# Optimization experiments

Measured on AMD Instinct MI355X. Metric: run time of the kernel, lower is better.

Reference implementation:

```python
import jax, jax.numpy as jnp
import numpy as np

B, T, D = 4, 2048, 1024
F = 4 * D  # Config.RWKV_INTERMIDATE_SIZE * hidden_dim
LN_EPS = 1e-3  # keras LayerNormalization default epsilon


def layer_norm(x, g, b, eps=LN_EPS):
    mu = jnp.mean(x, axis=-1, keepdims=True)
    var = jnp.mean(jnp.square(x - mu), axis=-1, keepdims=True)
    return (x - mu) * jax.lax.rsqrt(var + eps) * g + b


def setup_inputs() -> dict:
    ks = jax.random.split(jax.random.key(0), 24)
    g = lambda k, shape: (jax.random.normal(k, shape, jnp.float32)
                          * np.sqrt(2.0 / sum(shape)))  # ~glorot
    return {
        "x": jax.random.normal(ks[0], (B, T, D), jnp.float32),
        "s_cm": jnp.zeros((B, D), jnp.float32),
        "s_tm": jnp.zeros((B, D), jnp.float32),
        "s_num": jnp.zeros((B, D), jnp.float32),
        "s_den": jnp.zeros((B, D), jnp.float32),
        "s_q": jnp.zeros((B, D), jnp.float32),
        "ln1_g": jnp.ones((D,), jnp.float32),
        "ln1_b": jnp.zeros((D,), jnp.float32),
        "ln2_g": jnp.ones((D,), jnp.float32),
        "ln2_b": jnp.zeros((D,), jnp.float32),
        "tm_mix_k": jax.random.uniform(ks[1], (D,), jnp.float32, 0.0, 2.0 / D),
        "tm_mix_v": jax.random.uniform(ks[2], (D,), jnp.float32, 0.0, 2.0 / D),
        "tm_mix_r": jax.random.uniform(ks[3], (D,), jnp.float32, 0.0, (2.0 / D) ** 0.5),
        "tm_kw": g(ks[4], (D, D)),
        "tm_vw": g(ks[5], (D, D)),
        "tm_rw": g(ks[6], (D, D)),
        "time_decay": jax.random.uniform(ks[7], (D,), jnp.float32, 0.0, 0.1),
        "time_first": jax.random.uniform(ks[8], (D,), jnp.float32, 0.0, 0.05),
        "out_w": g(ks[9], (D, D)),
        "cm_mix_k": jax.random.uniform(ks[10], (D,), jnp.float32, 0.0, 2.0 / D),
        "cm_mix_r": jax.random.uniform(ks[11], (D,), jnp.float32, 0.0, 2.0 / D),
        "cm_kw": g(ks[12], (D, F)),
        "cm_vw": g(ks[13], (F, D)),
        "cm_rw": g(ks[14], (D, D)),
    }


def _shift(h, s):
    # token shift: prepend last-token state, drop last timestep
    return jnp.concatenate([s[:, None, :], h[:, :-1, :]], axis=1)


def reference(x, s_cm, s_tm, s_num, s_den, s_q,
              ln1_g, ln1_b, ln2_g, ln2_b,
              tm_mix_k, tm_mix_v, tm_mix_r, tm_kw, tm_vw, tm_rw,
              time_decay, time_first, out_w,
              cm_mix_k, cm_mix_r, cm_kw, cm_vw, cm_rw):
    # ---- time mixing ----
    h = layer_norm(x, ln1_g, ln1_b)  # [B,T,D]
    hs = _shift(h, s_tm)
    xk = h * tm_mix_k + hs * (1.0 - tm_mix_k)
    xv = h * tm_mix_v + hs * (1.0 - tm_mix_v)
    xr = h * tm_mix_r + hs * (1.0 - tm_mix_r)
    k = xk @ tm_kw  # [B,T,D]
    v = xv @ tm_vw
    r = jax.nn.sigmoid(xr @ tm_rw)
    w = -jnp.exp(time_decay)  # [D]

    def step(carry, kv):
        num, den, q = carry
        kt, vt = kv  # [B,D]
        mo = jnp.maximum(q, kt + time_first)
        e1 = jnp.exp(q - mo)
        e2 = jnp.exp(kt + time_first - mo)
        out = (e1 * num + e2 * vt) / (e1 * den + e2)
        ms = jnp.maximum(q + w, kt)
        e1s = jnp.exp(q + w - ms)
        e2s = jnp.exp(kt - ms)
        return (e1s * num + e2s * vt, e1s * den + e2s, ms), out

    (num, den, q), wkv = jax.lax.scan(
        step, (s_num, s_den, s_q),
        (k.transpose(1, 0, 2), v.transpose(1, 0, 2)))
    wkv = wkv.transpose(1, 0, 2)  # [B,T,D]
    x = x + (r * wkv) @ out_w

    # ---- channel mixing ----
    h2 = layer_norm(x, ln2_g, ln2_b)
    hs2 = _shift(h2, s_cm)
    xk2 = h2 * cm_mix_k + hs2 * (1.0 - cm_mix_k)
    xr2 = h2 * cm_mix_r + hs2 * (1.0 - cm_mix_r)
    kv = jnp.square(jax.nn.relu(xk2 @ cm_kw)) @ cm_vw  # [B,T,F] -> [B,T,D]
    x = x + jax.nn.sigmoid(xr2 @ cm_rw) * kv

    # new state: (cm_inputs, tm_inputs, num, den, q)
    return x, h2[:, -1], h[:, -1], num, den, q
```

## Files before the change

### kernel.cpp

```cpp
#include <hip/hip_runtime.h>

typedef unsigned short ushort_t;
typedef __attribute__((ext_vector_type(8))) short short8;
typedef __attribute__((ext_vector_type(4))) float f32x4;

#define B_ 4
#define T_ 2048
#define D_ 1024
#define F_ 4096
#define M_ (B_*T_)
#define CH_ 64
#define NC_ (T_/CH_)

#define AS1 __attribute__((address_space(1)))
#define AS3 __attribute__((address_space(3)))

__device__ __forceinline__ ushort_t f2bf(float f) {
  union { float f; unsigned u; } a; a.f = f;
  unsigned r = a.u + 0x7FFFu + ((a.u >> 16) & 1u);
  return (ushort_t)(r >> 16);
}

__device__ __forceinline__ float bf2f(ushort_t u) {
  union { unsigned u; float f; } a; a.u = ((unsigned)u) << 16;
  return a.f;
}

__device__ __forceinline__ void gl_lds16(const void* g, void* l) {
  __builtin_amdgcn_global_load_lds((AS1 void*)(__UINTPTR_TYPE__)g,
                                   (AS3 void*)l, 16, 0, 0);
}

__device__ __forceinline__ void xcd_swz(int gx, int gy, int& bx, int& by, int& bz) {
  int lid = blockIdx.x + gx * (blockIdx.y + gy * blockIdx.z);
  int nwg = gx * gy * gridDim.z;
  int cpx = nwg >> 3;
  int L = (lid & 7) * cpx + (lid >> 3);
  by = L % gy;
  int t1 = L / gy;
  bx = t1 % gx;
  bz = t1 / gx;
}

__global__ __launch_bounds__(256) void tconv(const float* __restrict__ W,
                                             ushort_t* __restrict__ Wt,
                                             int K, int N) {
  __shared__ float tile[32][33];
  int tx = threadIdx.x, ty = threadIdx.y;
  int n0 = blockIdx.x * 32, k0 = blockIdx.y * 32;
  #pragma unroll
  for (int i = 0; i < 32; i += 8)
    tile[ty + i][tx] = W[(size_t)(k0 + ty + i) * N + n0 + tx];
  __syncthreads();
  #pragma unroll
  for (int i = 0; i < 32; i += 8)
    Wt[(size_t)(n0 + ty + i) * K + k0 + tx] = f2bf(tile[tx][ty + i]);
}

__global__ __launch_bounds__(256) void tconv5(const float* __restrict__ s0,
                                              const float* __restrict__ s1,
                                              const float* __restrict__ s2,
                                              const float* __restrict__ s3,
                                              const float* __restrict__ s4,
                                              ushort_t* __restrict__ d0,
                                              ushort_t* __restrict__ d1,
                                              ushort_t* __restrict__ d2,
                                              ushort_t* __restrict__ d3,
                                              ushort_t* __restrict__ d4) {
  __shared__ float tile[32][33];
  int z = blockIdx.z;
  const float* W = (z == 0) ? s0 : (z == 1) ? s1 : (z == 2) ? s2 : (z == 3) ? s3 : s4;
  ushort_t* Wt   = (z == 0) ? d0 : (z == 1) ? d1 : (z == 2) ? d2 : (z == 3) ? d3 : d4;
  int tx = threadIdx.x, ty = threadIdx.y;
  int n0 = blockIdx.x * 32, k0 = blockIdx.y * 32;
  #pragma unroll
  for (int i = 0; i < 32; i += 8)
    tile[ty + i][tx] = W[(size_t)(k0 + ty + i) * D_ + n0 + tx];
  __syncthreads();
  #pragma unroll
  for (int i = 0; i < 32; i += 8)
    Wt[(size_t)(n0 + ty + i) * D_ + k0 + tx] = f2bf(tile[tx][ty + i]);
}

#define MIX1(c, p, f) f2bf((c) * (f) + (p) * (1.0f - (f)))

template <int NOUT>
__global__ __launch_bounds__(256)
void ln_mix(const float* __restrict__ xin, const float* __restrict__ st,
            const float* __restrict__ g, const float* __restrict__ bb,
            const float* __restrict__ mk, const float* __restrict__ mv,
            const float* __restrict__ mr,
            ushort_t* __restrict__ ok, ushort_t* __restrict__ ov,
            ushort_t* __restrict__ orr, float* __restrict__ last) {
  int row = blockIdx.x;
  int t = row & (T_ - 1);
  int b = row >> 11;
  int tid = threadIdx.x;
  const bool pln = (t != 0);
  float4 vc = ((const float4*)(xin + (size_t)row * D_))[tid];
  float4 vp = pln ? ((const float4*)(xin + (size_t)(row - 1) * D_))[tid]
                  : ((const float4*)(st + (size_t)b * D_))[tid];
  float s0 = vc.x + vc.y + vc.z + vc.w;
  float s1 = vc.x * vc.x + vc.y * vc.y + vc.z * vc.z + vc.w * vc.w;
  float s2 = vp.x + vp.y + vp.z + vp.w;
  float s3 = vp.x * vp.x + vp.y * vp.y + vp.z * vp.z + vp.w * vp.w;
  #pragma unroll
  for (int o = 32; o > 0; o >>= 1) {
    s0 += __shfl_down(s0, o); s1 += __shfl_down(s1, o);
    s2 += __shfl_down(s2, o); s3 += __shfl_down(s3, o);
  }
  __shared__ float red[4][4];
  if ((tid & 63) == 0) {
    int w = tid >> 6;
    red[w][0] = s0; red[w][1] = s1; red[w][2] = s2; red[w][3] = s3;
  }
  __syncthreads();
  float cs0 = red[0][0] + red[1][0] + red[2][0] + red[3][0];
  float cs1 = red[0][1] + red[1][1] + red[2][1] + red[3][1];
  float ps0 = red[0][2] + red[1][2] + red[2][2] + red[3][2];
  float ps1 = red[0][3] + red[1][3] + red[2][3] + red[3][3];

  float mu = cs0 * (1.0f / D_);
  float rs = rsqrtf(cs1 * (1.0f / D_) - mu * mu + 1e-3f);
  float4 gv = ((const float4*)g)[tid];
  float4 bv = ((const float4*)bb)[tid];
  float hc[4], hp[4];
  hc[0] = (vc.x - mu) * rs * gv.x + bv.x;
  hc[1] = (vc.y - mu) * rs * gv.y + bv.y;
  hc[2] = (vc.z - mu) * rs * gv.z + bv.z;
  hc[3] = (vc.w - mu) * rs * gv.w + bv.w;
  if (pln) {
    float mup = ps0 * (1.0f / D_);
    float rsp = rsqrtf(ps1 * (1.0f / D_) - mup * mup + 1e-3f);
    hp[0] = (vp.x - mup) * rsp * gv.x + bv.x;
    hp[1] = (vp.y - mup) * rsp * gv.y + bv.y;
    hp[2] = (vp.z - mup) * rsp * gv.z + bv.z;
    hp[3] = (vp.w - mup) * rsp * gv.w + bv.w;
  } else {
    hp[0] = vp.x; hp[1] = vp.y; hp[2] = vp.z; hp[3] = vp.w;
  }

  size_t qi = (size_t)row * 256 + tid;
  float4 k4 = ((const float4*)mk)[tid];
  float4 r4 = ((const float4*)mr)[tid];
  ushort4 o4;
  o4.x = MIX1(hc[0], hp[0], k4.x); o4.y = MIX1(hc[1], hp[1], k4.y);
  o4.z = MIX1(hc[2], hp[2], k4.z); o4.w = MIX1(hc[3], hp[3], k4.w);
  ((ushort4*)ok)[qi] = o4;
  if (NOUT == 3) {
    float4 v4 = ((const float4*)mv)[tid];
    o4.x = MIX1(hc[0], hp[0], v4.x); o4.y = MIX1(hc[1], hp[1], v4.y);
    o4.z = MIX1(hc[2], hp[2], v4.z); o4.w = MIX1(hc[3], hp[3], v4.w);
    ((ushort4*)ov)[qi] = o4;
  }
  o4.x = MIX1(hc[0], hp[0], r4.x); o4.y = MIX1(hc[1], hp[1], r4.y);
  o4.z = MIX1(hc[2], hp[2], r4.z); o4.w = MIX1(hc[3], hp[3], r4.w);
  ((ushort4*)orr)[qi] = o4;

  if (t == T_ - 1) {
    float4 h4; h4.x = hc[0]; h4.y = hc[1]; h4.z = hc[2]; h4.w = hc[3];
    ((float4*)(last + (size_t)b * D_))[tid] = h4;
  }
}

__global__ __launch_bounds__(256) void wkv_part1(const ushort_t* __restrict__ k,
                                                 const ushort_t* __restrict__ v,
                                                 const float* __restrict__ tdec,
                                                 float* __restrict__ cn,
                                                 float* __restrict__ cd,
                                                 float* __restrict__ cq) {
  int idx = blockIdx.x * 256 + threadIdx.x;
  int d = idx & (D_ - 1);
  int b = (idx >> 10) & (B_ - 1);
  int c = idx >> 12;
  float w = -__expf(tdec[d]);
  const ushort_t* kp = k + ((size_t)b * T_ + c * CH_) * D_ + d;
  const ushort_t* vp = v + ((size_t)b * T_ + c * CH_) * D_ + d;
  float num = 0.0f, den = 0.0f, q = -1e30f;
  for (int t0 = 0; t0 < CH_; t0 += 8) {
    float kt[8], vt[8];
    #pragma unroll
    for (int i = 0; i < 8; ++i) {
      size_t off = (size_t)(t0 + i) * D_;
      kt[i] = bf2f(kp[off]); vt[i] = bf2f(vp[off]);
    }
    #pragma unroll
    for (int i = 0; i < 8; ++i) {
      float kk = kt[i];
      float ms = fmaxf(q + w, kk);
      float e1 = __expf(q + w - ms), e2 = __expf(kk - ms);
      num = e1 * num + e2 * vt[i];
      den = e1 * den + e2;
      q = ms;
    }
  }
  cn[idx] = num; cd[idx] = den; cq[idx] = q;
}

__global__ __launch_bounds__(256) void wkv_part2(const float* __restrict__ cn,
                                                 const float* __restrict__ cd,
                                                 const float* __restrict__ cq,
                                                 const float* __restrict__ sn,
                                                 const float* __restrict__ sd,
                                                 const float* __restrict__ sq,
                                                 const float* __restrict__ tdec,
                                                 float* __restrict__ pn,
                                                 float* __restrict__ pd,
                                                 float* __restrict__ pq,
                                                 float* __restrict__ on,
                                                 float* __restrict__ od,
                                                 float* __restrict__ oq) {
  int idx = blockIdx.x * 256 + threadIdx.x;
  int d = idx & (D_ - 1);
  float w = -__expf(tdec[d]);
  float wL = w * (float)CH_;
  float num = sn[idx], den = sd[idx], q = sq[idx];
  #pragma unroll 4
  for (int c = 0; c < NC_; ++c) {
    int j = (c << 12) + idx;
    pn[j] = num; pd[j] = den; pq[j] = q;
    float m2 = cq[j];
    float qn = fmaxf(q + wL, m2);
    float e1 = __expf(q + wL - qn), e2 = __expf(m2 - qn);
    num = e1 * num + e2 * cn[j];
    den = e1 * den + e2 * cd[j];
    q = qn;
  }
  on[idx] = num; od[idx] = den; oq[idx] = q;
}

__global__ __launch_bounds__(256) void wkv_part3(const ushort_t* __restrict__ k,
                                                 const ushort_t* __restrict__ v,
                                                 const ushort_t* __restrict__ r,
                                                 const float* __restrict__ pn,
                                                 const float* __restrict__ pd,
                                                 const float* __restrict__ pq,
                                                 const float* __restrict__ tdec,
                                                 const float* __restrict__ tfirst,
                                                 ushort_t* __restrict__ rwkv) {
  int idx = blockIdx.x * 256 + threadIdx.x;
  int d = idx & (D_ - 1);
  int b = (idx >> 10) & (B_ - 1);
  int c = idx >> 12;
  float w = -__expf(tdec[d]);
  float tf = tfirst[d];
  float num = pn[idx], den = pd[idx], q = pq[idx];
  size_t base = ((size_t)b * T_ + c * CH_) * D_ + d;
  const ushort_t* kp = k + base;
  const ushort_t* vp = v + base;
  const ushort_t* rp = r + base;
  ushort_t* op = rwkv + base;
  for (int t0 = 0; t0 < CH_; t0 += 8) {
    float kt[8], vt[8], rt[8];
    #pragma unroll
    for (int i = 0; i < 8; ++i) {
      size_t off = (size_t)(t0 + i) * D_;
      kt[i] = bf2f(kp[off]); vt[i] = bf2f(vp[off]); rt[i] = bf2f(rp[off]);
    }
    #pragma unroll
    for (int i = 0; i < 8; ++i) {
      float kk = kt[i];
      float mo = fmaxf(q, kk + tf);
      float e1 = __expf(q - mo), e2 = __expf(kk + tf - mo);
      float o = (e1 * num + e2 * vt[i]) / (e1 * den + e2);
      op[(size_t)(t0 + i) * D_] = f2bf(rt[i] * o);
      float ms = fmaxf(q + w, kk);
      float e1s = __expf(q + w - ms), e2s = __expf(kk - ms);
      num = e1s * num + e2s * vt[i];
      den = e1s * den + e2s;
      q = ms;
    }
  }
}

template <int EPI>
__global__ __launch_bounds__(512, 2)
void gemm256(const ushort_t* __restrict__ A, const ushort_t* __restrict__ Bt,
             int N, int K, int ktn, ushort_t* __restrict__ Cb) {
  __shared__ alignas(16) ushort_t sA[2][256 * 64];
  __shared__ alignas(16) ushort_t sB[2][256 * 64];
  const int tid = threadIdx.x;
  const int lane = tid & 63;
  const int wave = tid >> 6;
  const int wr = wave >> 2, wc = wave & 3;
  const int l15 = lane & 15;
  const int kb = (lane >> 4) << 4;
  int bx, by, bz;
  xcd_swz(gridDim.x, gridDim.y, bx, by, bz);
  const int m0 = bx * 256, n0 = by * 256;
  const ushort_t* gA = A + (size_t)m0 * K;
  const ushort_t* gB = Bt + (size_t)n0 * K;

  const int sr = tid >> 3;
  const int sc8 = (tid & 7) ^ (sr & 7);
  const int scb = (tid & 7) * 16;

  auto stage = [&](int dbuf, int kt, int h) {
    const ushort_t* g = (h < 2) ? gA : gB;
    ushort_t* sb = (h < 2) ? sA[dbuf] : sB[dbuf];
    int rbase = (h & 1) * 128;
    #pragma unroll
    for (int i = 0; i < 2; ++i) {
      int row = rbase + i * 64 + sr;
      gl_lds16(g + (size_t)row * K + (size_t)kt * 64 + sc8 * 8,
               (char*)sb + row * 128 + scb);
    }
  };

  auto ld = [&](const ushort_t* sbuf, int row, int s5) -> short8 {
    int cb = ((s5 << 6) + kb) ^ ((row & 7) << 4);
    return *(const short8*)((const char*)sbuf + row * 128 + cb);
  };

  f32x4 acc[8][4] = {};

  stage(0, 0, 0); stage(0, 0, 1); stage(0, 0, 2); stage(0, 0, 3);

  for (int t = 0; t < ktn; ++t) {
    const int cur = t & 1, nxt = cur ^ 1;
    const bool more = (t + 1 < ktn);
    if (more) { stage(nxt, t + 1, 0); stage(nxt, t + 1, 1); }
    if (more) asm volatile("s_waitcnt vmcnt(4)" ::: "memory");
    else      asm volatile("s_waitcnt vmcnt(0)" ::: "memory");
    __builtin_amdgcn_s_barrier();

    const ushort_t* curA = sA[cur];
    const ushort_t* curB = sB[cur];
    short8 bfr[4][2];

#define G256_MFMA16(MI0, A00, A01, A10, A11)                                  \
    __builtin_amdgcn_s_setprio(1);                                            \
    _Pragma("unroll")                                                         \
    for (int ni = 0; ni < 4; ++ni) {                                          \
      acc[MI0][ni] = __builtin_amdgcn_mfma_f32_16x16x32_bf16(                 \
          A00, bfr[ni][0], acc[MI0][ni], 0, 0, 0);                            \
      acc[MI0][ni] = __builtin_amdgcn_mfma_f32_16x16x32_bf16(                 \
          A01, bfr[ni][1], acc[MI0][ni], 0, 0, 0);                            \
      acc[MI0 + 1][ni] = __builtin_amdgcn_mfma_f32_16x16x32_bf16(             \
          A10, bfr[ni][0], acc[MI0 + 1][ni], 0, 0, 0);                        \
      acc[MI0 + 1][ni] = __builtin_amdgcn_mfma_f32_16x16x32_bf16(             \
          A11, bfr[ni][1], acc[MI0 + 1][ni], 0, 0, 0);                        \
    }                                                                         \
    __builtin_amdgcn_s_setprio(0);

#define G256_SYNC_IN()                                                        \
    asm volatile("" ::: "memory");                                            \
    __builtin_amdgcn_s_barrier();                                             \
    asm volatile("s_waitcnt lgkmcnt(0)" ::: "memory");                        \
    __builtin_amdgcn_sched_barrier(0);

#define G256_SYNC_OUT()                                                       \
    asm volatile("" ::: "memory");                                            \
    __builtin_amdgcn_s_barrier();

    {
      #pragma unroll
      for (int ni = 0; ni < 4; ++ni)
        #pragma unroll
        for (int s = 0; s < 2; ++s)
          bfr[ni][s] = ld(curB, wc * 64 + ni * 16 + l15, s);
      short8 a00 = ld(curA, wr * 128 + 0 * 16 + l15, 0);
      short8 a01 = ld(curA, wr * 128 + 0 * 16 + l15, 1);
      short8 a10 = ld(curA, wr * 128 + 1 * 16 + l15, 0);
      short8 a11 = ld(curA, wr * 128 + 1 * 16 + l15, 1);
      if (more) stage(nxt, t + 1, 2);
      G256_SYNC_IN();
      G256_MFMA16(0, a00, a01, a10, a11);
      G256_SYNC_OUT();
    }
    {
      short8 a00 = ld(curA, wr * 128 + 2 * 16 + l15, 0);
      short8 a01 = ld(curA, wr * 128 + 2 * 16 + l15, 1);
      short8 a10 = ld(curA, wr * 128 + 3 * 16 + l15, 0);
      short8 a11 = ld(curA, wr * 128 + 3 * 16 + l15, 1);
      if (more) stage(nxt, t + 1, 3);
      G256_SYNC_IN();
      G256_MFMA16(2, a00, a01, a10, a11);
      G256_SYNC_OUT();
    }
    {
      short8 a00 = ld(curA, wr * 128 + 4 * 16 + l15, 0);
      short8 a01 = ld(curA, wr * 128 + 4 * 16 + l15, 1);
      short8 a10 = ld(curA, wr * 128 + 5 * 16 + l15, 0);
      short8 a11 = ld(curA, wr * 128 + 5 * 16 + l15, 1);
      G256_SYNC_IN();
      G256_MFMA16(4, a00, a01, a10, a11);
      G256_SYNC_OUT();
    }
    {
      short8 a00 = ld(curA, wr * 128 + 6 * 16 + l15, 0);
      short8 a01 = ld(curA, wr * 128 + 6 * 16 + l15, 1);
      short8 a10 = ld(curA, wr * 128 + 7 * 16 + l15, 0);
      short8 a11 = ld(curA, wr * 128 + 7 * 16 + l15, 1);
      G256_SYNC_IN();
      G256_MFMA16(6, a00, a01, a10, a11);
      G256_SYNC_OUT();
    }
  }

  #pragma unroll
  for (int mi = 0; mi < 8; ++mi)
    #pragma unroll
    for (int ni = 0; ni < 4; ++ni)
      #pragma unroll
      for (int j = 0; j < 4; ++j) {
        int row = m0 + wr * 128 + mi * 16 + ((lane >> 4) << 2) + j;
        int col = n0 + wc * 64 + ni * 16 + l15;
        size_t idx = (size_t)row * N + col;
        float v = acc[mi][ni][j];
        float tt = v > 0.0f ? v : 0.0f;
        Cb[idx] = f2bf(tt * tt);
      }
}

template <int EPI>
__global__ __launch_bounds__(512, 2)
void gemmB(const ushort_t* __restrict__ A, const ushort_t* __restrict__ Bt,
           int K, int ktn,
           float* __restrict__ Cf, ushort_t* __restrict__ Ub,
           const float* __restrict__ X, const float* __restrict__ X2) {
  __shared__ alignas(16) ushort_t sA[2][128 * 64];
  __shared__ alignas(16) ushort_t sB[2][256 * 64];
  const int tid = threadIdx.x;
  const int lane = tid & 63;
  const int wave = tid >> 6;
  const int wr = wave >> 2, wc = wave & 3;
  const int l15 = lane & 15;
  const int kb = (lane >> 4) << 4;
  int bx, by, zid;
  xcd_swz(gridDim.x, gridDim.y, bx, by, zid);
  const int m0 = bx * 128, n0 = by * 256;

  const ushort_t* Ause = A;
  const ushort_t* Buse = Bt;
  if (EPI == 3) {
    Ause = A + (size_t)zid * M_ * D_;
    Buse = Bt + (size_t)zid * D_ * D_;
  }
  const ushort_t* gA = Ause + (size_t)m0 * K;
  const ushort_t* gB = Buse + (size_t)n0 * K;

  const int sr = tid >> 3;
  const int sc8 = (tid & 7) ^ (sr & 7);
  const int scb = (tid & 7) * 16;

  auto stage = [&](int dbuf, int kt, int h) {
    if (h < 2) {
      int row = h * 64 + sr;
      gl_lds16(gA + (size_t)row * K + (size_t)kt * 64 + sc8 * 8,
               (char*)sA[dbuf] + row * 128 + scb);
    } else {
      int rbase = (h - 2) * 128;
      #pragma unroll
      for (int i = 0; i < 2; ++i) {
        int row = rbase + i * 64 + sr;
        gl_lds16(gB + (size_t)row * K + (size_t)kt * 64 + sc8 * 8,
                 (char*)sB[dbuf] + row * 128 + scb);
      }
    }
  };

  auto ld = [&](const ushort_t* sbuf, int row, int s5) -> short8 {
    int cb = ((s5 << 6) + kb) ^ ((row & 7) << 4);
    return *(const short8*)((const char*)sbuf + row * 128 + cb);
  };

  f32x4 acc[4][4] = {};

  stage(0, 0, 0); stage(0, 0, 1); stage(0, 0, 2); stage(0, 0, 3);

  for (int t = 0; t < ktn; ++t) {
    const int cur = t & 1, nxt = cur ^ 1;
    const bool more = (t + 1 < ktn);
    if (more) {
      stage(nxt, t + 1, 0); stage(nxt, t + 1, 1);
      stage(nxt, t + 1, 2); stage(nxt, t + 1, 3);
    }
    if (more) asm volatile("s_waitcnt vmcnt(6)" ::: "memory");
    else      asm volatile("s_waitcnt vmcnt(0)" ::: "memory");
    __builtin_amdgcn_s_barrier();

    const ushort_t* curA = sA[cur];
    const ushort_t* curB = sB[cur];

    #pragma unroll
    for (int s = 0; s < 2; ++s) {
      short8 av[4], bv[4];
      #pragma unroll
      for (int i = 0; i < 4; ++i) av[i] = ld(curA, wr * 64 + i * 16 + l15, s);
      #pragma unroll
      for (int i = 0; i < 4; ++i) bv[i] = ld(curB, wc * 64 + i * 16 + l15, s);
      asm volatile("" ::: "memory");
      __builtin_amdgcn_s_barrier();
      asm volatile("s_waitcnt lgkmcnt(0)" ::: "memory");
      __builtin_amdgcn_sched_barrier(0);
      __builtin_amdgcn_s_setprio(1);
      #pragma unroll
      for (int mi = 0; mi < 4; ++mi)
        #pragma unroll
        for (int ni = 0; ni < 4; ++ni)
          acc[mi][ni] = __builtin_amdgcn_mfma_f32_16x16x32_bf16(
              av[mi], bv[ni], acc[mi][ni], 0, 0, 0);
      __builtin_amdgcn_s_setprio(0);
      asm volatile("" ::: "memory");
      __builtin_amdgcn_s_barrier();
    }
  }

  ushort_t* ub = (EPI == 3) ? Ub + (size_t)zid * M_ * D_ : nullptr;
  #pragma unroll
  for (int mi = 0; mi < 4; ++mi)
    #pragma unroll
    for (int ni = 0; ni < 4; ++ni)
      #pragma unroll
      for (int j = 0; j < 4; ++j) {
        int row = m0 + wr * 64 + mi * 16 + ((lane >> 4) << 2) + j;
        int col = n0 + wc * 64 + ni * 16 + l15;
        size_t idx = (size_t)row * D_ + col;
        float v = acc[mi][ni][j];
        if (EPI == 2) {
          Cf[idx] = X[idx] + v;
        } else if (EPI == 3) {
          if (zid == 2) v = 1.0f / (1.0f + __expf(-v));
          ub[idx] = f2bf(v);
        } else if (EPI == 4) {
          float s = 1.0f / (1.0f + __expf(-v));
          Cf[idx] = X2[idx] + s * X[idx];
        } else if (EPI == 5) {
          Cf[idx] = v;
        }
      }
}

extern "C" void kernel_launch(void* const* d_in, const int* in_sizes, int n_in,
                              void* d_out, int out_size, void* d_ws, size_t ws_size,
                              hipStream_t stream) {
  const float* x      = (const float*)d_in[0];
  const float* s_cm   = (const float*)d_in[1];
  const float* s_tm   = (const float*)d_in[2];
  const float* s_num  = (const float*)d_in[3];
  const float* s_den  = (const float*)d_in[4];
  const float* s_q    = (const float*)d_in[5];
  const float* ln1_g  = (const float*)d_in[6];
  const float* ln1_b  = (const float*)d_in[7];
  const float* ln2_g  = (const float*)d_in[8];
  const float* ln2_b  = (const float*)d_in[9];
  const float* tmk    = (const float*)d_in[10];
  const float* tmv    = (const float*)d_in[11];
  const float* tmr    = (const float*)d_in[12];
  const float* tm_kw  = (const float*)d_in[13];
  const float* tm_vw  = (const float*)d_in[14];
  const float* tm_rw  = (const float*)d_in[15];
  const float* tdec   = (const float*)d_in[16];
  const float* tfirst = (const float*)d_in[17];
  const float* out_w  = (const float*)d_in[18];
  const float* cmk    = (const float*)d_in[19];
  const float* cmr    = (const float*)d_in[20];
  const float* cm_kw  = (const float*)d_in[21];
  const float* cm_vw  = (const float*)d_in[22];
  const float* cm_rw  = (const float*)d_in[23];

  float* out   = (float*)d_out;
  float* o_x   = out;
  float* o_h2l = out + (size_t)M_ * D_;
  float* o_hl  = o_h2l + B_ * D_;
  float* o_num = o_hl + B_ * D_;
  float* o_den = o_num + B_ * D_;
  float* o_q   = o_den + B_ * D_;

  char* W = (char*)d_ws;
  const size_t MB = 1024 * 1024;
  ushort_t* w_tmk = (ushort_t*)(W + 0 * MB);
  ushort_t* w_tmv = (ushort_t*)(W + 2 * MB);
  ushort_t* w_tmr = (ushort_t*)(W + 4 * MB);
  ushort_t* w_out = (ushort_t*)(W + 6 * MB);
  ushort_t* w_cmk = (ushort_t*)(W + 8 * MB);
  ushort_t* w_cmv = (ushort_t*)(W + 16 * MB);
  ushort_t* w_cmr = (ushort_t*)(W + 24 * MB);
  float* cn = (float*)(W + 26 * MB + 0 * 512 * 1024);
  float* cd = (float*)(W + 26 * MB + 1 * 512 * 1024);
  float* cq = (float*)(W + 26 * MB + 2 * 512 * 1024);
  float* pn = (float*)(W + 26 * MB + 3 * 512 * 1024);
  float* pd = (float*)(W + 26 * MB + 4 * 512 * 1024);
  float* pq = (float*)(W + 26 * MB + 5 * 512 * 1024);
  ushort_t* xk    = (ushort_t*)(W + 32 * MB);
  ushort_t* xv    = (ushort_t*)(W + 48 * MB);
  ushort_t* xr    = (ushort_t*)(W + 64 * MB);
  ushort_t* kbuf  = (ushort_t*)(W + 80 * MB);
  ushort_t* vbuf  = (ushort_t*)(W + 96 * MB);
  ushort_t* rbuf  = (ushort_t*)(W + 112 * MB);
  ushort_t* kk    = (ushort_t*)(W + 128 * MB);
  float*    kv    = (float*)(W + 80 * MB);
  ushort_t* rwkv  = xr;
  ushort_t* xk2   = xk;
  ushort_t* xr2   = xv;

  dim3 tb(32, 8);
  tconv5<<<dim3(D_/32, D_/32, 5), tb, 0, stream>>>(tm_kw, tm_vw, tm_rw, out_w, cm_rw,
                                                   w_tmk, w_tmv, w_tmr, w_out, w_cmr);
  tconv<<<dim3(F_/32, D_/32), tb, 0, stream>>>(cm_kw, w_cmk, D_, F_);
  tconv<<<dim3(D_/32, F_/32), tb, 0, stream>>>(cm_vw, w_cmv, F_, D_);

  ln_mix<3><<<M_, 256, 0, stream>>>(x, s_tm, ln1_g, ln1_b, tmk, tmv, tmr,
                                    xk, xv, xr, o_hl);
  gemmB<3><<<dim3(M_/128, D_/256, 3), 512, 0, stream>>>(
      xk, w_tmk, D_, D_/64, nullptr, kbuf, nullptr, nullptr);

  wkv_part1<<<(NC_ * B_ * D_) / 256, 256, 0, stream>>>(kbuf, vbuf, tdec, cn, cd, cq);
  wkv_part2<<<(B_ * D_) / 256, 256, 0, stream>>>(cn, cd, cq, s_num, s_den, s_q, tdec,
                                                 pn, pd, pq, o_num, o_den, o_q);
  wkv_part3<<<(NC_ * B_ * D_) / 256, 256, 0, stream>>>(kbuf, vbuf, rbuf, pn, pd, pq,
                                                       tdec, tfirst, rwkv);

  gemmB<2><<<dim3(M_/128, D_/256, 1), 512, 0, stream>>>(
      rwkv, w_out, D_, D_/64, o_x, nullptr, x, nullptr);

  ln_mix<2><<<M_, 256, 0, stream>>>(o_x, s_cm, ln2_g, ln2_b, cmk, nullptr, cmr,
                                    xk2, nullptr, xr2, o_h2l);
  gemm256<1><<<dim3(M_/256, F_/256, 1), 512, 0, stream>>>(
      xk2, w_cmk, F_, D_, D_/64, kk);
  gemmB<5><<<dim3(M_/128, D_/256, 1), 512, 0, stream>>>(
      kk, w_cmv, F_, F_/64, kv, nullptr, nullptr, nullptr);
  gemmB<4><<<dim3(M_/128, D_/256, 1), 512, 0, stream>>>(
      xr2, w_cmr, D_, D_/64, o_x, nullptr, kv, o_x);
}
```

Measured before the change: 429.0 us.

## Move QKV and down-projection GEMMs to 256x256 tiles with split-K

The batched k/v/r projection moves from the 128x256 GEMM onto the larger 256x256 tile kernel. The F->D down-projection now runs as a 2-way split-K on 256x256 tiles, writing two fp32 partial buffers. The final sigmoid-gate epilogue sums both partials. The goal is more data reuse per tile and enough blocks to fill the GPU despite the larger tiles. The cost is an extra fp32 partial write and read, and the workspace buffers are reused differently.

```diff
diff --git a/kernel.cpp b/kernel.cpp
--- a/kernel.cpp
+++ b/kernel.cpp
@@ -276,7 +276,9 @@
 template <int EPI>
 __global__ __launch_bounds__(512, 2)
 void gemm256(const ushort_t* __restrict__ A, const ushort_t* __restrict__ Bt,
-             int N, int K, int ktn, ushort_t* __restrict__ Cb) {
+             int N, int K, int ktn,
+             float* __restrict__ Cf, float* __restrict__ Cf2,
+             ushort_t* __restrict__ Ub) {
   __shared__ alignas(16) ushort_t sA[2][256 * 64];
   __shared__ alignas(16) ushort_t sB[2][256 * 64];
   const int tid = threadIdx.x;
@@ -288,8 +290,16 @@
   int bx, by, bz;
   xcd_swz(gridDim.x, gridDim.y, bx, by, bz);
   const int m0 = bx * 256, n0 = by * 256;
-  const ushort_t* gA = A + (size_t)m0 * K;
-  const ushort_t* gB = Bt + (size_t)n0 * K;
+  const int kt0 = (EPI == 0) ? bz * ktn : 0;
+
+  const ushort_t* Ause = A;
+  const ushort_t* Buse = Bt;
+  if (EPI == 3) {
+    Ause = A + (size_t)bz * M_ * D_;
+    Buse = Bt + (size_t)bz * D_ * D_;
+  }
+  const ushort_t* gA = Ause + (size_t)m0 * K + (size_t)kt0 * 64;
+  const ushort_t* gB = Buse + (size_t)n0 * K + (size_t)kt0 * 64;
 
   const int sr = tid >> 3;
   const int sc8 = (tid & 7) ^ (sr & 7);
@@ -398,6 +408,9 @@
     }
   }
 
+  float* cfp = (EPI == 0 && bz) ? Cf2 : Cf;
+  ushort_t* ub = Ub;
+  if (EPI == 3) ub = Ub + (size_t)bz * M_ * D_;
   #pragma unroll
   for (int mi = 0; mi < 8; ++mi)
     #pragma unroll
@@ -408,8 +421,15 @@
         int col = n0 + wc * 64 + ni * 16 + l15;
         size_t idx = (size_t)row * N + col;
         float v = acc[mi][ni][j];
-        float tt = v > 0.0f ? v : 0.0f;
-        Cb[idx] = f2bf(tt * tt);
+        if (EPI == 0) {
+          cfp[idx] = v;
+        } else if (EPI == 1) {
+          float tt = v > 0.0f ? v : 0.0f;
+          ub[idx] = f2bf(tt * tt);
+        } else if (EPI == 3) {
+          if (bz == 2) v = 1.0f / (1.0f + __expf(-v));
+          ub[idx] = f2bf(v);
+        }
       }
 }
 
@@ -417,8 +437,9 @@
 __global__ __launch_bounds__(512, 2)
 void gemmB(const ushort_t* __restrict__ A, const ushort_t* __restrict__ Bt,
            int K, int ktn,
-           float* __restrict__ Cf, ushort_t* __restrict__ Ub,
-           const float* __restrict__ X, const float* __restrict__ X2) {
+           float* __restrict__ Cf,
+           const float* __restrict__ X, const float* __restrict__ X2,
+           const float* __restrict__ Xb) {
   __shared__ alignas(16) ushort_t sA[2][128 * 64];
   __shared__ alignas(16) ushort_t sB[2][256 * 64];
   const int tid = threadIdx.x;
@@ -431,14 +452,8 @@
   xcd_swz(gridDim.x, gridDim.y, bx, by, zid);
   const int m0 = bx * 128, n0 = by * 256;
 
-  const ushort_t* Ause = A;
-  const ushort_t* Buse = Bt;
-  if (EPI == 3) {
-    Ause = A + (size_t)zid * M_ * D_;
-    Buse = Bt + (size_t)zid * D_ * D_;
-  }
-  const ushort_t* gA = Ause + (size_t)m0 * K;
-  const ushort_t* gB = Buse + (size_t)n0 * K;
+  const ushort_t* gA = A + (size_t)m0 * K;
+  const ushort_t* gB = Bt + (size_t)n0 * K;
 
   const int sr = tid >> 3;
   const int sc8 = (tid & 7) ^ (sr & 7);
@@ -507,7 +522,6 @@
     }
   }
 
-  ushort_t* ub = (EPI == 3) ? Ub + (size_t)zid * M_ * D_ : nullptr;
   #pragma unroll
   for (int mi = 0; mi < 4; ++mi)
     #pragma unroll
@@ -520,14 +534,9 @@
         float v = acc[mi][ni][j];
         if (EPI == 2) {
           Cf[idx] = X[idx] + v;
-        } else if (EPI == 3) {
-          if (zid == 2) v = 1.0f / (1.0f + __expf(-v));
-          ub[idx] = f2bf(v);
         } else if (EPI == 4) {
           float s = 1.0f / (1.0f + __expf(-v));
-          Cf[idx] = X2[idx] + s * X[idx];
-        } else if (EPI == 5) {
-          Cf[idx] = v;
+          Cf[idx] = X2[idx] + s * (X[idx] + Xb[idx]);
         }
       }
 }
@@ -590,7 +599,8 @@
   ushort_t* vbuf  = (ushort_t*)(W + 96 * MB);
   ushort_t* rbuf  = (ushort_t*)(W + 112 * MB);
   ushort_t* kk    = (ushort_t*)(W + 128 * MB);
-  float*    kv    = (float*)(W + 80 * MB);
+  float*    kv_a  = (float*)(W + 64 * MB);
+  float*    kv_b  = (float*)(W + 96 * MB);
   ushort_t* rwkv  = xr;
   ushort_t* xk2   = xk;
   ushort_t* xr2   = xv;
@@ -603,8 +613,8 @@
 
   ln_mix<3><<<M_, 256, 0, stream>>>(x, s_tm, ln1_g, ln1_b, tmk, tmv, tmr,
                                     xk, xv, xr, o_hl);
-  gemmB<3><<<dim3(M_/128, D_/256, 3), 512, 0, stream>>>(
-      xk, w_tmk, D_, D_/64, nullptr, kbuf, nullptr, nullptr);
+  gemm256<3><<<dim3(M_/256, D_/256, 3), 512, 0, stream>>>(
+      xk, w_tmk, D_, D_, D_/64, nullptr, nullptr, kbuf);
 
   wkv_part1<<<(NC_ * B_ * D_) / 256, 256, 0, stream>>>(kbuf, vbuf, tdec, cn, cd, cq);
   wkv_part2<<<(B_ * D_) / 256, 256, 0, stream>>>(cn, cd, cq, s_num, s_den, s_q, tdec,
@@ -613,14 +623,14 @@
                                                        tdec, tfirst, rwkv);
 
   gemmB<2><<<dim3(M_/128, D_/256, 1), 512, 0, stream>>>(
-      rwkv, w_out, D_, D_/64, o_x, nullptr, x, nullptr);
+      rwkv, w_out, D_, D_/64, o_x, x, nullptr, nullptr);
 
   ln_mix<2><<<M_, 256, 0, stream>>>(o_x, s_cm, ln2_g, ln2_b, cmk, nullptr, cmr,
                                     xk2, nullptr, xr2, o_h2l);
   gemm256<1><<<dim3(M_/256, F_/256, 1), 512, 0, stream>>>(
-      xk2, w_cmk, F_, D_, D_/64, kk);
-  gemmB<5><<<dim3(M_/128, D_/256, 1), 512, 0, stream>>>(
-      kk, w_cmv, F_, F_/64, kv, nullptr, nullptr, nullptr);
+      xk2, w_cmk, F_, D_, D_/64, nullptr, nullptr, kk);
+  gemm256<0><<<dim3(M_/256, D_/256, 2), 512, 0, stream>>>(
+      kk, w_cmv, D_, F_, F_/128, kv_a, kv_b, nullptr);
   gemmB<4><<<dim3(M_/128, D_/256, 1), 512, 0, stream>>>(
-      xr2, w_cmr, D_, D_/64, o_x, nullptr, kv, o_x);
-}
+      xr2, w_cmr, D_, D_/64, o_x, kv_a, o_x, kv_b);
+}
```

Result: faster. 407.0 us (-5.1%).
